# Kernel tuning notes

Hardware: AMD Instinct MI355X
Metric: run time of the kernel (lower is better)

## Reference

```python
import jax, jax.numpy as jnp
import numpy as np
from jax import lax

NEURON_CDECAY = 0.0
NEURON_VDECAY = 0.75
NEURON_VTH = 0.5
SPIKE_WINDOW = 0.5


@jax.custom_vjp
def pseudo_spike(v):
    return (v > NEURON_VTH).astype(v.dtype)

def _ps_fwd(v):
    return pseudo_spike(v), v

def _ps_bwd(v, g):
    grad = (jnp.abs(v - NEURON_VTH) < SPIKE_WINDOW).astype(g.dtype)
    return (g * grad,)

pseudo_spike.defvjp(_ps_fwd, _ps_bwd)


def setup_inputs() -> dict:
    key = jax.random.key(0)
    ks = jax.random.split(key, 8)
    B, D_IN, T = 2048, 1024, 64
    H1, H2, D_OUT = 512, 512, 512
    # binary input spikes, like population-encoded Poisson spikes
    in_pop_spikes = (jax.random.uniform(ks[0], (B, D_IN, T)) < 0.5).astype(jnp.float32)
    def lin(kw, kb, fan_out, fan_in):
        bound = 1.0 / np.sqrt(fan_in)
        W = jax.random.uniform(kw, (fan_out, fan_in), minval=-bound, maxval=bound, dtype=jnp.float32)
        b = jax.random.uniform(kb, (fan_out,), minval=-bound, maxval=bound, dtype=jnp.float32)
        return W, b
    W1, b1 = lin(ks[1], ks[2], H1, D_IN)
    W2, b2 = lin(ks[3], ks[4], H2, H1)
    Wout, bout = lin(ks[5], ks[6], D_OUT, H2)
    return {"in_pop_spikes": in_pop_spikes, "W1": W1, "b1": b1,
            "W2": W2, "b2": b2, "Wout": Wout, "bout": bout,
            "batch_size": B}


def reference(in_pop_spikes, W1, b1, W2, b2, Wout, bout, batch_size):
    B = batch_size
    H1, H2 = W1.shape[0], W2.shape[0]
    dt = in_pop_spikes.dtype
    # [T, B, D_in]
    xs = jnp.transpose(in_pop_spikes, (2, 0, 1))
    z1 = jnp.zeros((B, H1), dt)
    z2 = jnp.zeros((B, H2), dt)
    init = (z1, z1, z1, z2, z2, z2, z2)  # c1,v1,s1,c2,v2,s2,acc

    def step(carry, x_t):
        c1, v1, s1, c2, v2, s2, acc = carry
        c1 = c1 * NEURON_CDECAY + x_t @ W1.T + b1
        v1 = v1 * (1.0 - s1) * NEURON_VDECAY + c1
        s1 = pseudo_spike(v1)
        c2 = c2 * NEURON_CDECAY + s1 @ W2.T + b2
        v2 = v2 * (1.0 - s2) * NEURON_VDECAY + c2
        s2 = pseudo_spike(v2)
        acc = acc + s2
        return (c1, v1, s1, c2, v2, s2, acc), None

    carry, _ = lax.scan(step, init, xs)
    out_pop_act = carry[-1]
    return out_pop_act @ Wout.T + bout
```

## Files before the change

### kernel.cpp

```cpp
#include <hip/hip_runtime.h>
#include <hip/hip_bf16.h>
#include <type_traits>

typedef int  i32x4  __attribute__((ext_vector_type(4)));
typedef int  i32x16 __attribute__((ext_vector_type(16)));
typedef unsigned int uint;
typedef unsigned long long u64;

constexpr int TN = 64;
constexpr float W_INV  = 1.1920928955078125e-7f;
constexpr float WO_INV = 5.9604644775390625e-8f;

static constexpr size_t OFF_XP2 = (size_t)16 << 20;
static constexpr size_t OFF_W1  = (size_t)24 << 20;
static constexpr size_t OFF_W2  = OFF_W1 + (size_t)3 * 4 * 16 * 8192;
static constexpr size_t OFF_WO  = OFF_W2 + (size_t)3 * 4 * 8 * 8192;
static constexpr size_t WS_NEED = OFF_WO + (size_t)3 * 512 * 512;

__global__ __launch_bounds__(256) void pack_x(const float* __restrict__ X,
                                              u64* __restrict__ XP) {
    __shared__ float L[64 * 65];
    const int kw = blockIdx.x;
    const int b  = blockIdx.y;
    const int tid = threadIdx.x;
    const float* src = X + (((size_t)b * 1024 + kw * 64) << 6);
#pragma unroll
    for (int i = 0; i < 4; ++i) {
        int flat = tid + i * 256;
        float4 v = ((const float4*)src)[flat];
        int e0 = flat * 4;
        int k = e0 >> 6, t0 = e0 & 63;
        float* d = &L[k * 65 + t0];
        d[0] = v.x; d[1] = v.y; d[2] = v.z; d[3] = v.w;
    }
    __syncthreads();
    const int w = tid >> 6, lane = tid & 63;
    u64 myw = 0;
#pragma unroll
    for (int tt = 0; tt < 16; ++tt) {
        int t = w * 16 + tt;
        bool pred = L[lane * 65 + t] > 0.5f;
        u64 bm = __ballot(pred);
        if (lane == tt) myw = bm;
    }
    if (lane < 16) XP[((size_t)b * 16 + kw) * 64 + w * 16 + lane] = myw;
}

__global__ __launch_bounds__(256) void pack_w3(const float* __restrict__ W, int kshift, int KB,
                                               char* __restrict__ dAll) {
    int g = blockIdx.x * 256 + threadIdx.x;
    int h = g >> kshift;
    int k = g & ((1 << kshift) - 1);
    float v = W[g];
    int q  = (int)rintf(v * 8388608.f);
    int lo = ((q + 64) & 127) - 64;
    int q1 = (q - lo) >> 7;
    int mid = ((q1 + 64) & 127) - 64;
    int hi  = (q1 - mid) >> 7;
    size_t tile0 = (size_t)((h >> 7) * KB + (k >> 6)) * 8192;
    size_t inT   = (size_t)(h & 127) * 64 + (k & 63);
    size_t compStride = (size_t)4 * KB * 8192;
    dAll[tile0 + inT]                  = (char)hi;
    dAll[compStride + tile0 + inT]     = (char)mid;
    dAll[2 * compStride + tile0 + inT] = (char)lo;
}

__global__ __launch_bounds__(256) void pack_wout3(const float* __restrict__ W,
                                                  char* __restrict__ dAll) {
    int g = blockIdx.x * 256 + threadIdx.x;
    float v = W[g];
    int q  = (int)rintf(v * 16777216.f);
    int lo = ((q + 64) & 127) - 64;
    int q1 = (q - lo) >> 7;
    int mid = ((q1 + 64) & 127) - 64;
    int hi  = (q1 - mid) >> 7;
    dAll[g]          = (char)hi;
    dAll[262144 + g] = (char)mid;
    dAll[524288 + g] = (char)lo;
}

template <int KB, bool EMIT>
__global__ __launch_bounds__(256, 2) void spike_mfma_v4(
    const char* __restrict__ dAll,
    const void* __restrict__ XPsrc,
    const float* __restrict__ bias,
    uint* __restrict__ XPdst,
    char* __restrict__ AccOut)
{
    __shared__ float LS[4][64 * 33];
    const int tid = threadIdx.x;
    const int nb = blockIdx.x, hy = blockIdx.y;
    const int b0 = nb * 2;
    const int w = tid >> 6, lane = tid & 63;
    const int wm = w >> 1, wn = w & 1;
    const int l31 = lane & 31, lh = lane >> 5;
    const int bsel = b0 + wn;

    i32x16 acc[3][2] = {};

    const char* aBase = dAll + (size_t)(hy >> 1) * KB * 8192
                        + ((hy & 1) * 64 + wm * 32 + l31) * 64 + lh * 16;
    const size_t dStride = (size_t)4 * KB * 8192;

    const u64*  xp64 = (const u64*)XPsrc  + (size_t)bsel * KB * 64 + l31;
    const uint* xp32 = (const uint*)XPsrc + (size_t)bsel * 1024 + l31;

    uint4 aC[3][2], aN[3][2];
    u64  b64C[2] = {}, b64N[2] = {};
    uint b32C[4] = {}, b32N[4] = {};

    auto loadA = [&](int kb, uint4 (&dst)[3][2]) {
#pragma unroll
        for (int d = 0; d < 3; ++d)
#pragma unroll
            for (int ks = 0; ks < 2; ++ks)
                dst[d][ks] = *(const uint4*)(aBase + d * dStride + (size_t)kb * 8192 + ks * 32);
    };
    auto loadB = [&](int kb, u64 (&d64)[2], uint (&d32)[4]) {
        if constexpr (EMIT) {
#pragma unroll
            for (int ni = 0; ni < 2; ++ni)
                d64[ni] = xp64[(size_t)kb * 64 + ni * 32];
        } else {
#pragma unroll
            for (int ni = 0; ni < 2; ++ni)
#pragma unroll
                for (int ks = 0; ks < 2; ++ks)
                    d32[ni * 2 + ks] = xp32[(size_t)(kb * 2 + ks) * 64 + ni * 32];
        }
    };

    loadA(0, aC);
    loadB(0, b64C, b32C);

#pragma unroll 2
    for (int kb = 0; kb < KB; ++kb) {
        const int kbn = (kb + 1 < KB) ? kb + 1 : KB - 1;
        loadA(kbn, aN);
        loadB(kbn, b64N, b32N);
        __builtin_amdgcn_s_setprio(1);
#pragma unroll
        for (int ni = 0; ni < 2; ++ni)
#pragma unroll
            for (int ks = 0; ks < 2; ++ks) {
                uint f;
                if constexpr (EMIT)
                    f = (uint)(b64C[ni] >> (ks * 32 + lh * 16)) & 0xFFFFu;
                else
                    f = (b32C[ni * 2 + ks] >> (lh * 16)) & 0xFFFFu;
                i32x4 bf;
                bf[0] = (int)((((f      ) & 15u) * 0x204081u) & 0x01010101u);
                bf[1] = (int)((((f >>  4) & 15u) * 0x204081u) & 0x01010101u);
                bf[2] = (int)((((f >>  8) & 15u) * 0x204081u) & 0x01010101u);
                bf[3] = (int)((((f >> 12) & 15u) * 0x204081u) & 0x01010101u);
#pragma unroll
                for (int d = 0; d < 3; ++d)
                    acc[d][ni] = __builtin_amdgcn_mfma_i32_32x32x32_i8(
                        __builtin_bit_cast(i32x4, aC[d][ks]), bf, acc[d][ni], 0, 0, 0);
            }
        __builtin_amdgcn_s_setprio(0);
#pragma unroll
        for (int d = 0; d < 3; ++d) { aC[d][0] = aN[d][0]; aC[d][1] = aN[d][1]; }
        b64C[0] = b64N[0]; b64C[1] = b64N[1];
        b32C[0] = b32N[0]; b32C[1] = b32N[1]; b32C[2] = b32N[2]; b32C[3] = b32N[3];
    }

    float* myLS = LS[w];
#pragma unroll
    for (int ni = 0; ni < 2; ++ni) {
        const int t = ni * 32 + l31;
#pragma unroll
        for (int q = 0; q < 4; ++q)
#pragma unroll
            for (int j = 0; j < 4; ++j) {
                int r = q * 4 + j;
                int comb = (acc[0][ni][r] << 14) + (acc[1][ni][r] << 7) + acc[2][ni][r];
                myLS[t * 33 + q * 8 + lh * 4 + j] = (float)comb * W_INV;
            }
    }
    asm volatile("s_waitcnt lgkmcnt(0)" ::: "memory");
    __builtin_amdgcn_sched_barrier(0);
    if (lane < 32) {
        const float bb = bias[hy * 64 + wm * 32 + lane];
        float v = 0.f, s = 0.f;
        uint w0 = 0, w1 = 0;
        int asum = 0;
        for (int tt = 0; tt < TN; ++tt) {
            float cc = myLS[tt * 33 + lane] + bb;
            v = v * (1.f - s) * 0.75f + cc;
            bool sp = v > 0.5f;
            s = sp ? 1.f : 0.f;
            if constexpr (EMIT) {
                u64 bm = __ballot(sp);
                if (lane == (tt & 31)) { if (tt < 32) w0 = (uint)bm; else w1 = (uint)bm; }
            } else {
                asum += sp ? 1 : 0;
            }
        }
        if constexpr (EMIT) {
            uint base = ((uint)bsel * 16 + hy * 2 + wm) * 64;
            XPdst[base + lane] = w0;
            XPdst[base + 32 + lane] = w1;
        } else {
            AccOut[(size_t)bsel * 512 + hy * 64 + wm * 32 + lane] = (char)asum;
        }
    }
}

__global__ __launch_bounds__(256) void k3_i8(
    const char* __restrict__ dW,
    const char* __restrict__ ACCb,
    const float* __restrict__ bq,
    float* __restrict__ out)
{
    const int tid = threadIdx.x;
    const int w = tid >> 6, lane = tid & 63;
    const int l31 = lane & 31, lh = lane >> 5;
    const int bBlk = blockIdx.x * 64;
    const int oBase = blockIdx.y * 128 + w * 32;

    i32x16 acc[2][3] = {};
    const char* aP = dW + (size_t)(oBase + l31) * 512 + lh * 16;
    const char* bP = ACCb + (size_t)(bBlk + l31) * 512 + lh * 16;

#pragma unroll 4
    for (int ks = 0; ks < 16; ++ks) {
        i32x4 af[3], bf[2];
#pragma unroll
        for (int d = 0; d < 3; ++d)
            af[d] = *(const i32x4*)(aP + (size_t)d * 262144 + ks * 32);
#pragma unroll
        for (int bi = 0; bi < 2; ++bi)
            bf[bi] = *(const i32x4*)(bP + (size_t)bi * 32 * 512 + ks * 32);
#pragma unroll
        for (int bi = 0; bi < 2; ++bi)
#pragma unroll
            for (int d = 0; d < 3; ++d)
                acc[bi][d] = __builtin_amdgcn_mfma_i32_32x32x32_i8(af[d], bf[bi], acc[bi][d], 0, 0, 0);
    }
#pragma unroll
    for (int bi = 0; bi < 2; ++bi) {
        const size_t b = bBlk + bi * 32 + l31;
#pragma unroll
        for (int q = 0; q < 4; ++q) {
            const int oo = oBase + q * 8 + lh * 4;
            float4 bb = *(const float4*)&bq[oo];
            float4 o4;
#pragma unroll
            for (int j = 0; j < 4; ++j) {
                int r = q * 4 + j;
                float dv = (float)acc[bi][0][r] * 16384.f
                         + (float)acc[bi][1][r] * 128.f
                         + (float)acc[bi][2][r];
                ((float*)&o4)[j] = dv * WO_INV + ((const float*)&bb)[j];
            }
            *(float4*)&out[b * 512 + oo] = o4;
        }
    }
}

template <int KDIM, bool PIN>
__global__ __launch_bounds__(256) void gemm_scan(
    const float* __restrict__ Xf, const u64* __restrict__ Xp,
    const float* __restrict__ W, const float* __restrict__ bias,
    u64* __restrict__ Sout, float* __restrict__ AccOut) {
    __shared__ union {
        struct { float Wt[32 * 260]; float Xc[32 * 64]; } s;
        float C[256 * 64];
    } lds;
    const int b = blockIdx.y;
    const int h0 = blockIdx.x * 256;
    const int tid = threadIdx.x;
    const int tc = tid & 3, tr = tid >> 2;
    const int t0 = tc * 16, r0 = tr * 4;
    float c[4][16];
#pragma unroll
    for (int i = 0; i < 4; ++i)
#pragma unroll
        for (int j = 0; j < 16; ++j) c[i][j] = 0.f;
    for (int k0 = 0; k0 < KDIM; k0 += 32) {
        if constexpr (!PIN) {
            const float4* xsrc = (const float4*)(Xf + ((size_t)b * KDIM + k0) * 64);
            float4* xdst = (float4*)lds.s.Xc;
            xdst[tid] = xsrc[tid];
            xdst[tid + 256] = xsrc[tid + 256];
        } else {
            const int row = tid >> 3;
            const int bofs = (tid & 7) * 8;
            u64 m = Xp[(size_t)b * KDIM + k0 + row];
            float* xd = &lds.s.Xc[row * 64 + bofs];
#pragma unroll
            for (int q = 0; q < 8; ++q) xd[q] = (float)((m >> (bofs + q)) & 1ull);
        }
#pragma unroll
        for (int i = 0; i < 8; ++i) {
            int g = tid + 256 * i;
            int row = g >> 3, c4 = g & 7;
            float4 w4 = *(const float4*)(W + (size_t)(h0 + row) * KDIM + k0 + c4 * 4);
            lds.s.Wt[(c4 * 4 + 0) * 260 + row] = w4.x;
            lds.s.Wt[(c4 * 4 + 1) * 260 + row] = w4.y;
            lds.s.Wt[(c4 * 4 + 2) * 260 + row] = w4.z;
            lds.s.Wt[(c4 * 4 + 3) * 260 + row] = w4.w;
        }
        __syncthreads();
#pragma unroll 4
        for (int kk = 0; kk < 32; ++kk) {
            float4 wv = *(const float4*)&lds.s.Wt[kk * 260 + r0];
            const float4* xr = (const float4*)&lds.s.Xc[kk * 64 + t0];
            float4 x0 = xr[0], x1 = xr[1], x2 = xr[2], x3 = xr[3];
            float wr[4] = {wv.x, wv.y, wv.z, wv.w};
            float xs[16] = {x0.x, x0.y, x0.z, x0.w, x1.x, x1.y, x1.z, x1.w,
                            x2.x, x2.y, x2.z, x2.w, x3.x, x3.y, x3.z, x3.w};
#pragma unroll
            for (int i = 0; i < 4; ++i)
#pragma unroll
                for (int j = 0; j < 16; ++j) c[i][j] = fmaf(wr[i], xs[j], c[i][j]);
        }
        __syncthreads();
    }
#pragma unroll
    for (int i = 0; i < 4; ++i)
#pragma unroll
        for (int j4 = 0; j4 < 4; ++j4)
            *(float4*)&lds.C[(r0 + i) * 64 + t0 + j4 * 4] =
                make_float4(c[i][j4 * 4], c[i][j4 * 4 + 1], c[i][j4 * 4 + 2], c[i][j4 * 4 + 3]);
    __syncthreads();
    const float bb = bias[h0 + tid];
    float v = 0.f, s = 0.f;
    if constexpr (!PIN) {
        u64 m = 0;
#pragma unroll
        for (int t = 0; t < TN; ++t) {
            float cc = lds.C[tid * 64 + t] + bb;
            v = v * (1.f - s) * 0.75f + cc;
            bool sp = v > 0.5f;
            s = sp ? 1.f : 0.f;
            if (sp) m |= (1ull << t);
        }
        Sout[(size_t)b * 512 + h0 + tid] = m;
    } else {
        float acc = 0.f;
#pragma unroll
        for (int t = 0; t < TN; ++t) {
            float cc = lds.C[tid * 64 + t] + bb;
            v = v * (1.f - s) * 0.75f + cc;
            bool sp = v > 0.5f;
            s = sp ? 1.f : 0.f;
            acc += s;
        }
        AccOut[(size_t)b * 512 + h0 + tid] = acc;
    }
}

__global__ __launch_bounds__(256) void k3_f32(
    const float* __restrict__ A, const float* __restrict__ Wo,
    const float* __restrict__ bq, float* __restrict__ C) {
    __shared__ float Al[64][33];
    __shared__ float Bl[32][65];
    const int n0 = blockIdx.x * 64;
    const int m0 = blockIdx.y * 64;
    const int tid = threadIdx.x;
    const int c0 = (tid & 15) * 4;
    const int r0 = (tid >> 4) * 4;
    float acc[4][4];
#pragma unroll
    for (int i = 0; i < 4; ++i)
#pragma unroll
        for (int j = 0; j < 4; ++j) acc[i][j] = 0.f;
    for (int k0 = 0; k0 < 512; k0 += 32) {
#pragma unroll
        for (int i = 0; i < 2; ++i) {
            int g = tid + 256 * i;
            int row = g >> 3, c4 = g & 7;
            float4 v = *(const float4*)(A + (size_t)(m0 + row) * 512 + k0 + c4 * 4);
            float* d = &Al[row][c4 * 4];
            d[0] = v.x; d[1] = v.y; d[2] = v.z; d[3] = v.w;
        }
#pragma unroll
        for (int i = 0; i < 2; ++i) {
            int g = tid + 256 * i;
            int row = g >> 3, c4 = g & 7;
            float4 v = *(const float4*)(Wo + (size_t)(n0 + row) * 512 + k0 + c4 * 4);
            Bl[c4 * 4 + 0][row] = v.x; Bl[c4 * 4 + 1][row] = v.y;
            Bl[c4 * 4 + 2][row] = v.z; Bl[c4 * 4 + 3][row] = v.w;
        }
        __syncthreads();
#pragma unroll 8
        for (int kk = 0; kk < 32; ++kk) {
            float a0 = Al[r0 + 0][kk], a1 = Al[r0 + 1][kk];
            float a2 = Al[r0 + 2][kk], a3 = Al[r0 + 3][kk];
            float b0 = Bl[kk][c0 + 0], b1 = Bl[kk][c0 + 1];
            float b2 = Bl[kk][c0 + 2], b3 = Bl[kk][c0 + 3];
            acc[0][0] = fmaf(a0, b0, acc[0][0]); acc[0][1] = fmaf(a0, b1, acc[0][1]);
            acc[0][2] = fmaf(a0, b2, acc[0][2]); acc[0][3] = fmaf(a0, b3, acc[0][3]);
            acc[1][0] = fmaf(a1, b0, acc[1][0]); acc[1][1] = fmaf(a1, b1, acc[1][1]);
            acc[1][2] = fmaf(a1, b2, acc[1][2]); acc[1][3] = fmaf(a1, b3, acc[1][3]);
            acc[2][0] = fmaf(a2, b0, acc[2][0]); acc[2][1] = fmaf(a2, b1, acc[2][1]);
            acc[2][2] = fmaf(a2, b2, acc[2][2]); acc[2][3] = fmaf(a2, b3, acc[2][3]);
            acc[3][0] = fmaf(a3, b0, acc[3][0]); acc[3][1] = fmaf(a3, b1, acc[3][1]);
            acc[3][2] = fmaf(a3, b2, acc[3][2]); acc[3][3] = fmaf(a3, b3, acc[3][3]);
        }
        __syncthreads();
    }
#pragma unroll
    for (int i = 0; i < 4; ++i) {
        float4 o = make_float4(acc[i][0] + bq[n0 + c0 + 0], acc[i][1] + bq[n0 + c0 + 1],
                               acc[i][2] + bq[n0 + c0 + 2], acc[i][3] + bq[n0 + c0 + 3]);
        *(float4*)&C[(size_t)(m0 + r0 + i) * 512 + n0 + c0] = o;
    }
}

extern "C" void kernel_launch(void* const* d_in, const int* in_sizes, int n_in,
                              void* d_out, int out_size, void* d_ws, size_t ws_size,
                              hipStream_t stream) {
    const float* X  = (const float*)d_in[0];
    const float* W1 = (const float*)d_in[1];
    const float* b1 = (const float*)d_in[2];
    const float* W2 = (const float*)d_in[3];
    const float* b2 = (const float*)d_in[4];
    const float* Wo = (const float*)d_in[5];
    const float* bo = (const float*)d_in[6];
    float* out = (float*)d_out;

    if (ws_size >= WS_NEED) {
        char* ws = (char*)d_ws;
        u64* XPk1 = (u64*)ws;
        uint* XP2 = (uint*)(ws + OFF_XP2);
        char* W1d = ws + OFF_W1;
        char* W2d = ws + OFF_W2;
        char* WoD = ws + OFF_WO;
        char* ACCb = ws;

        pack_x<<<dim3(16, 2048), 256, 0, stream>>>(X, XPk1);
        pack_w3<<<dim3(2048), 256, 0, stream>>>(W1, 10, 16, W1d);
        pack_w3<<<dim3(1024), 256, 0, stream>>>(W2, 9, 8, W2d);
        pack_wout3<<<dim3(1024), 256, 0, stream>>>(Wo, WoD);
        spike_mfma_v4<16, true><<<dim3(1024, 8), 256, 0, stream>>>(W1d, XPk1, b1, XP2, nullptr);
        spike_mfma_v4<8, false><<<dim3(1024, 8), 256, 0, stream>>>(W2d, XP2, b2, nullptr, ACCb);
        k3_i8<<<dim3(32, 4), 256, 0, stream>>>(WoD, ACCb, bo, out);
    } else {
        u64* S1 = (u64*)d_ws;
        float* ACC = (float*)((char*)d_ws + (size_t)2048 * 512 * 8);
        gemm_scan<1024, false><<<dim3(2, 2048), 256, 0, stream>>>(X, nullptr, W1, b1, S1, nullptr);
        gemm_scan<512, true><<<dim3(2, 2048), 256, 0, stream>>>(nullptr, S1, W2, b2, nullptr, ACC);
        k3_f32<<<dim3(8, 32), 256, 0, stream>>>(ACC, Wo, bo, out);
    }
}
```

Measured before the change: 450.3 us.

## Stage weight tiles through double-buffered LDS shared across waves

Result: slower. 733.1 us (+62.8%).

```diff
diff --git a/kernel.cpp b/kernel.cpp
--- a/kernel.cpp
+++ b/kernel.cpp
@@ -57,12 +57,15 @@
     int q1 = (q - lo) >> 7;
     int mid = ((q1 + 64) & 127) - 64;
     int hi  = (q1 - mid) >> 7;
-    size_t tile0 = (size_t)((h >> 7) * KB + (k >> 6)) * 8192;
-    size_t inT   = (size_t)(h & 127) * 64 + (k & 63);
-    size_t compStride = (size_t)4 * KB * 8192;
-    dAll[tile0 + inT]                  = (char)hi;
-    dAll[compStride + tile0 + inT]     = (char)mid;
-    dAll[2 * compStride + tile0 + inT] = (char)lo;
+    size_t plane = (size_t)32768 * KB;
+    int hy = h >> 6, wm = (h >> 5) & 1, row = h & 31;
+    int kb = k >> 6, ks = (k >> 5) & 1, lhp = (k >> 4) & 1, kbyte = k & 15;
+    size_t off = ((size_t)(hy * KB + kb)) * 4096
+               + (size_t)(((wm * 2 + ks) * 2 + lhp) * 512)
+               + row * 16 + kbyte;
+    dAll[off]             = (char)hi;
+    dAll[plane + off]     = (char)mid;
+    dAll[2 * plane + off] = (char)lo;
 }
 
 __global__ __launch_bounds__(256) void pack_wout3(const float* __restrict__ W,
@@ -80,14 +83,15 @@
 }
 
 template <int KB, bool EMIT>
-__global__ __launch_bounds__(256, 2) void spike_mfma_v4(
+__global__ __launch_bounds__(256, 2) void spike_mfma_v5(
     const char* __restrict__ dAll,
     const void* __restrict__ XPsrc,
     const float* __restrict__ bias,
     uint* __restrict__ XPdst,
     char* __restrict__ AccOut)
 {
-    __shared__ float LS[4][64 * 33];
+    constexpr size_t PLANE = (size_t)32768 * KB;
+    __shared__ __align__(16) char smem[33792];
     const int tid = threadIdx.x;
     const int nb = blockIdx.x, hy = blockIdx.y;
     const int b0 = nb * 2;
@@ -98,24 +102,15 @@
 
     i32x16 acc[3][2] = {};
 
-    const char* aBase = dAll + (size_t)(hy >> 1) * KB * 8192
-                        + ((hy & 1) * 64 + wm * 32 + l31) * 64 + lh * 16;
-    const size_t dStride = (size_t)4 * KB * 8192;
+    const char* tileBase = dAll + (size_t)hy * KB * 4096;
 
     const u64*  xp64 = (const u64*)XPsrc  + (size_t)bsel * KB * 64 + l31;
     const uint* xp32 = (const uint*)XPsrc + (size_t)bsel * 1024 + l31;
 
-    uint4 aC[3][2], aN[3][2];
     u64  b64C[2] = {}, b64N[2] = {};
     uint b32C[4] = {}, b32N[4] = {};
-
-    auto loadA = [&](int kb, uint4 (&dst)[3][2]) {
-#pragma unroll
-        for (int d = 0; d < 3; ++d)
-#pragma unroll
-            for (int ks = 0; ks < 2; ++ks)
-                dst[d][ks] = *(const uint4*)(aBase + d * dStride + (size_t)kb * 8192 + ks * 32);
-    };
+    uint4 ga[3];
+
     auto loadB = [&](int kb, u64 (&d64)[2], uint (&d32)[4]) {
         if constexpr (EMIT) {
 #pragma unroll
@@ -129,15 +124,37 @@
                     d32[ni * 2 + ks] = xp32[(size_t)(kb * 2 + ks) * 64 + ni * 32];
         }
     };
-
-    loadA(0, aC);
+    auto loadGA = [&](int kb) {
+#pragma unroll
+        for (int d = 0; d < 3; ++d)
+            ga[d] = *(const uint4*)(tileBase + d * PLANE + (size_t)kb * 4096 + tid * 16);
+    };
+    auto writeGA = [&](char* buf) {
+#pragma unroll
+        for (int d = 0; d < 3; ++d)
+            *(uint4*)(buf + d * 4096 + tid * 16) = ga[d];
+    };
+
+    loadGA(0);
     loadB(0, b64C, b32C);
+    writeGA(smem);
+    __syncthreads();
 
 #pragma unroll 2
     for (int kb = 0; kb < KB; ++kb) {
-        const int kbn = (kb + 1 < KB) ? kb + 1 : KB - 1;
-        loadA(kbn, aN);
-        loadB(kbn, b64N, b32N);
+        char* bufC = smem + (kb & 1) * 12288;
+        char* bufN = smem + ((kb + 1) & 1) * 12288;
+        if (kb + 1 < KB) {
+            loadGA(kb + 1);
+            loadB(kb + 1, b64N, b32N);
+        }
+        i32x4 af[3][2];
+#pragma unroll
+        for (int d = 0; d < 3; ++d)
+#pragma unroll
+            for (int ks = 0; ks < 2; ++ks)
+                af[d][ks] = *(const i32x4*)(bufC + d * 4096
+                              + ((wm * 2 + ks) * 2 + lh) * 512 + l31 * 16);
         __builtin_amdgcn_s_setprio(1);
 #pragma unroll
         for (int ni = 0; ni < 2; ++ni)
@@ -156,16 +173,16 @@
 #pragma unroll
                 for (int d = 0; d < 3; ++d)
                     acc[d][ni] = __builtin_amdgcn_mfma_i32_32x32x32_i8(
-                        __builtin_bit_cast(i32x4, aC[d][ks]), bf, acc[d][ni], 0, 0, 0);
+                        af[d][ks], bf, acc[d][ni], 0, 0, 0);
             }
         __builtin_amdgcn_s_setprio(0);
-#pragma unroll
-        for (int d = 0; d < 3; ++d) { aC[d][0] = aN[d][0]; aC[d][1] = aN[d][1]; }
+        if (kb + 1 < KB) writeGA(bufN);
+        __syncthreads();
         b64C[0] = b64N[0]; b64C[1] = b64N[1];
         b32C[0] = b32N[0]; b32C[1] = b32N[1]; b32C[2] = b32N[2]; b32C[3] = b32N[3];
     }
 
-    float* myLS = LS[w];
+    float* myLS = (float*)smem + w * (64 * 33);
 #pragma unroll
     for (int ni = 0; ni < 2; ++ni) {
         const int t = ni * 32 + l31;
@@ -435,8 +452,8 @@
         pack_w3<<<dim3(2048), 256, 0, stream>>>(W1, 10, 16, W1d);
         pack_w3<<<dim3(1024), 256, 0, stream>>>(W2, 9, 8, W2d);
         pack_wout3<<<dim3(1024), 256, 0, stream>>>(Wo, WoD);
-        spike_mfma_v4<16, true><<<dim3(1024, 8), 256, 0, stream>>>(W1d, XPk1, b1, XP2, nullptr);
-        spike_mfma_v4<8, false><<<dim3(1024, 8), 256, 0, stream>>>(W2d, XP2, b2, nullptr, ACCb);
+        spike_mfma_v5<16, true><<<dim3(1024, 8), 256, 0, stream>>>(W1d, XPk1, b1, XP2, nullptr);
+        spike_mfma_v5<8, false><<<dim3(1024, 8), 256, 0, stream>>>(W2d, XP2, b2, nullptr, ACCb);
         k3_i8<<<dim3(32, 4), 256, 0, stream>>>(WoD, ACCb, bo, out);
     } else {
         u64* S1 = (u64*)d_ws;
```

## Retile spike MFMA kernel so each wave covers both batch rows

Applied to the files above, without the earlier changes.

After: 409.3 us. 9.1% less time.

```diff
diff --git a/kernel.cpp b/kernel.cpp
--- a/kernel.cpp
+++ b/kernel.cpp
@@ -80,7 +80,7 @@
 }
 
 template <int KB, bool EMIT>
-__global__ __launch_bounds__(256, 2) void spike_mfma_v4(
+__global__ __launch_bounds__(256, 2) void spike_mfma_v6(
     const char* __restrict__ dAll,
     const void* __restrict__ XPsrc,
     const float* __restrict__ bias,
@@ -89,58 +89,55 @@
 {
     __shared__ float LS[4][64 * 33];
     const int tid = threadIdx.x;
-    const int nb = blockIdx.x, hy = blockIdx.y;
+    const int nb = blockIdx.x, hg = blockIdx.y;
     const int b0 = nb * 2;
     const int w = tid >> 6, lane = tid & 63;
-    const int wm = w >> 1, wn = w & 1;
+    const int wm = w;
     const int l31 = lane & 31, lh = lane >> 5;
-    const int bsel = b0 + wn;
-
-    i32x16 acc[3][2] = {};
-
-    const char* aBase = dAll + (size_t)(hy >> 1) * KB * 8192
-                        + ((hy & 1) * 64 + wm * 32 + l31) * 64 + lh * 16;
+
+    i32x16 acc[3][4] = {};
+
     const size_t dStride = (size_t)4 * KB * 8192;
-
-    const u64*  xp64 = (const u64*)XPsrc  + (size_t)bsel * KB * 64 + l31;
-    const uint* xp32 = (const uint*)XPsrc + (size_t)bsel * 1024 + l31;
-
-    uint4 aC[3][2], aN[3][2];
-    u64  b64C[2] = {}, b64N[2] = {};
-    uint b32C[4] = {}, b32N[4] = {};
-
-    auto loadA = [&](int kb, uint4 (&dst)[3][2]) {
+    const char* aBase = dAll + (size_t)hg * KB * 8192 + (wm * 32 + l31) * 64 + lh * 16;
+
+    const u64*  xp64a = (const u64*)XPsrc + (size_t)b0 * KB * 64 + l31;
+    const u64*  xp64b = xp64a + (size_t)KB * 64;
+    const uint* xp32a = (const uint*)XPsrc + (size_t)b0 * 1024 + l31;
+    const uint* xp32b = xp32a + 1024;
+
+    u64  b64C[4] = {}, b64N[4] = {};
+    uint b32C[8] = {}, b32N[8] = {};
+
+    auto loadB = [&](int kb, u64 (&d64)[4], uint (&d32)[8]) {
+        if constexpr (EMIT) {
+            d64[0] = xp64a[(size_t)kb * 64];
+            d64[1] = xp64a[(size_t)kb * 64 + 32];
+            d64[2] = xp64b[(size_t)kb * 64];
+            d64[3] = xp64b[(size_t)kb * 64 + 32];
+        } else {
+#pragma unroll
+            for (int th = 0; th < 2; ++th)
+#pragma unroll
+                for (int ks = 0; ks < 2; ++ks) {
+                    d32[(th    ) * 2 + ks] = xp32a[(size_t)(kb * 2 + ks) * 64 + th * 32];
+                    d32[(2 + th) * 2 + ks] = xp32b[(size_t)(kb * 2 + ks) * 64 + th * 32];
+                }
+        }
+    };
+
+    loadB(0, b64C, b32C);
+
+    for (int kb = 0; kb < KB; ++kb) {
+        i32x4 af[3][2];
 #pragma unroll
         for (int d = 0; d < 3; ++d)
 #pragma unroll
             for (int ks = 0; ks < 2; ++ks)
-                dst[d][ks] = *(const uint4*)(aBase + d * dStride + (size_t)kb * 8192 + ks * 32);
-    };
-    auto loadB = [&](int kb, u64 (&d64)[2], uint (&d32)[4]) {
-        if constexpr (EMIT) {
-#pragma unroll
-            for (int ni = 0; ni < 2; ++ni)
-                d64[ni] = xp64[(size_t)kb * 64 + ni * 32];
-        } else {
-#pragma unroll
-            for (int ni = 0; ni < 2; ++ni)
-#pragma unroll
-                for (int ks = 0; ks < 2; ++ks)
-                    d32[ni * 2 + ks] = xp32[(size_t)(kb * 2 + ks) * 64 + ni * 32];
-        }
-    };
-
-    loadA(0, aC);
-    loadB(0, b64C, b32C);
-
-#pragma unroll 2
-    for (int kb = 0; kb < KB; ++kb) {
-        const int kbn = (kb + 1 < KB) ? kb + 1 : KB - 1;
-        loadA(kbn, aN);
-        loadB(kbn, b64N, b32N);
+                af[d][ks] = *(const i32x4*)(aBase + d * dStride + (size_t)kb * 8192 + ks * 32);
+        if (kb + 1 < KB) loadB(kb + 1, b64N, b32N);
         __builtin_amdgcn_s_setprio(1);
 #pragma unroll
-        for (int ni = 0; ni < 2; ++ni)
+        for (int ni = 0; ni < 4; ++ni)
 #pragma unroll
             for (int ks = 0; ks < 2; ++ks) {
                 uint f;
@@ -156,53 +153,57 @@
 #pragma unroll
                 for (int d = 0; d < 3; ++d)
                     acc[d][ni] = __builtin_amdgcn_mfma_i32_32x32x32_i8(
-                        __builtin_bit_cast(i32x4, aC[d][ks]), bf, acc[d][ni], 0, 0, 0);
+                        af[d][ks], bf, acc[d][ni], 0, 0, 0);
             }
         __builtin_amdgcn_s_setprio(0);
 #pragma unroll
-        for (int d = 0; d < 3; ++d) { aC[d][0] = aN[d][0]; aC[d][1] = aN[d][1]; }
-        b64C[0] = b64N[0]; b64C[1] = b64N[1];
-        b32C[0] = b32N[0]; b32C[1] = b32N[1]; b32C[2] = b32N[2]; b32C[3] = b32N[3];
+        for (int i = 0; i < 4; ++i) b64C[i] = b64N[i];
+#pragma unroll
+        for (int i = 0; i < 8; ++i) b32C[i] = b32N[i];
     }
 
     float* myLS = LS[w];
 #pragma unroll
-    for (int ni = 0; ni < 2; ++ni) {
-        const int t = ni * 32 + l31;
-#pragma unroll
-        for (int q = 0; q < 4; ++q)
-#pragma unroll
-            for (int j = 0; j < 4; ++j) {
-                int r = q * 4 + j;
-                int comb = (acc[0][ni][r] << 14) + (acc[1][ni][r] << 7) + acc[2][ni][r];
-                myLS[t * 33 + q * 8 + lh * 4 + j] = (float)comb * W_INV;
+    for (int bi = 0; bi < 2; ++bi) {
+#pragma unroll
+        for (int th = 0; th < 2; ++th) {
+            const int ni = bi * 2 + th;
+            const int t = th * 32 + l31;
+#pragma unroll
+            for (int q = 0; q < 4; ++q)
+#pragma unroll
+                for (int j = 0; j < 4; ++j) {
+                    int r = q * 4 + j;
+                    int comb = (acc[0][ni][r] << 14) + (acc[1][ni][r] << 7) + acc[2][ni][r];
+                    myLS[t * 33 + q * 8 + lh * 4 + j] = (float)comb * W_INV;
+                }
+        }
+        asm volatile("s_waitcnt lgkmcnt(0)" ::: "memory");
+        __builtin_amdgcn_sched_barrier(0);
+        if (lane < 32) {
+            const float bb = bias[hg * 128 + wm * 32 + lane];
+            float v = 0.f, s = 0.f;
+            uint w0 = 0, w1 = 0;
+            int asum = 0;
+            for (int tt = 0; tt < TN; ++tt) {
+                float cc = myLS[tt * 33 + lane] + bb;
+                v = v * (1.f - s) * 0.75f + cc;
+                bool sp = v > 0.5f;
+                s = sp ? 1.f : 0.f;
+                if constexpr (EMIT) {
+                    u64 bm = __ballot(sp);
+                    if (lane == (tt & 31)) { if (tt < 32) w0 = (uint)bm; else w1 = (uint)bm; }
+                } else {
+                    asum += sp ? 1 : 0;
+                }
             }
-    }
-    asm volatile("s_waitcnt lgkmcnt(0)" ::: "memory");
-    __builtin_amdgcn_sched_barrier(0);
-    if (lane < 32) {
-        const float bb = bias[hy * 64 + wm * 32 + lane];
-        float v = 0.f, s = 0.f;
-        uint w0 = 0, w1 = 0;
-        int asum = 0;
-        for (int tt = 0; tt < TN; ++tt) {
-            float cc = myLS[tt * 33 + lane] + bb;
-            v = v * (1.f - s) * 0.75f + cc;
-            bool sp = v > 0.5f;
-            s = sp ? 1.f : 0.f;
             if constexpr (EMIT) {
-                u64 bm = __ballot(sp);
-                if (lane == (tt & 31)) { if (tt < 32) w0 = (uint)bm; else w1 = (uint)bm; }
+                uint base = ((uint)(b0 + bi) * 16 + hg * 4 + wm) * 64;
+                XPdst[base + lane] = w0;
+                XPdst[base + 32 + lane] = w1;
             } else {
-                asum += sp ? 1 : 0;
+                AccOut[(size_t)(b0 + bi) * 512 + hg * 128 + wm * 32 + lane] = (char)asum;
             }
-        }
-        if constexpr (EMIT) {
-            uint base = ((uint)bsel * 16 + hy * 2 + wm) * 64;
-            XPdst[base + lane] = w0;
-            XPdst[base + 32 + lane] = w1;
-        } else {
-            AccOut[(size_t)bsel * 512 + hy * 64 + wm * 32 + lane] = (char)asum;
         }
     }
 }
@@ -435,8 +436,8 @@
         pack_w3<<<dim3(2048), 256, 0, stream>>>(W1, 10, 16, W1d);
         pack_w3<<<dim3(1024), 256, 0, stream>>>(W2, 9, 8, W2d);
         pack_wout3<<<dim3(1024), 256, 0, stream>>>(Wo, WoD);
-        spike_mfma_v4<16, true><<<dim3(1024, 8), 256, 0, stream>>>(W1d, XPk1, b1, XP2, nullptr);
-        spike_mfma_v4<8, false><<<dim3(1024, 8), 256, 0, stream>>>(W2d, XP2, b2, nullptr, ACCb);
+        spike_mfma_v6<16, true><<<dim3(1024, 4), 256, 0, stream>>>(W1d, XPk1, b1, XP2, nullptr);
+        spike_mfma_v6<8, false><<<dim3(1024, 4), 256, 0, stream>>>(W2d, XP2, b2, nullptr, ACCb);
         k3_i8<<<dim3(32, 4), 256, 0, stream>>>(WoD, ACCb, bo, out);
     } else {
         u64* S1 = (u64*)d_ws;
```
